# Optimization experiments

Hardware: AMD Instinct MI355X
Metric: run time of the kernel (lower is better)

Reference implementation:

```python
import jax, jax.numpy as jnp
import numpy as np

N, K_, D_ = 16384, 32, 128

def setup_inputs() -> dict:
    key = jax.random.key(0)
    k1, k2, k3 = jax.random.split(key, 3)
    x = jax.random.normal(k1, (1, N, D_), dtype=jnp.float32)
    codes = jax.random.normal(k2, (K_, D_), dtype=jnp.float32)
    scale = jax.random.uniform(k3, (K_,), dtype=jnp.float32)
    return {"x": x, "codes": codes, "scale": scale}

def reference(x, codes, scale):
    # x: (1, N, D) -> residuals R: (N, K, D)
    R = x[0][:, None, :] - codes[None, :, :]
    # scaled L2 norm (NOT squared) over D, scaled per-codeword by `scale`
    l2 = jnp.linalg.norm(R, axis=-1)            # (N, K)
    W = jax.nn.softmax(l2 * scale, axis=-1)     # softmax over K
    # aggregated encoding: (K, D)
    E = jnp.einsum('nk,nkd->kd', W, R)
    return E
```

## Files before the change

kernel.cpp:

```cpp
#include <hip/hip_runtime.h>

constexpr int N    = 16384;
constexpr int K    = 32;
constexpr int D    = 128;
constexpr int SPAD = K + 4;

constexpr int ROWS1 = 32;
constexpr int GRID1 = N / ROWS1;

__global__ __launch_bounds__(256) void enc_partial(
    const float* __restrict__ x,
    const float* __restrict__ codes,
    const float* __restrict__ scale,
    float* __restrict__ ws)
{
    __shared__ float xs[ROWS1][D];
    __shared__ float sc_lds[ROWS1][SPAD];
    __shared__ float w_lds[ROWS1][SPAD];

    const int tid = threadIdx.x;
    const int k   = tid >> 3;
    const int dc  = tid & 7;
    const int d0  = dc << 4;

    {
        const float4* xg = reinterpret_cast<const float4*>(x + (long)blockIdx.x * ROWS1 * D);
        float4* xs4 = reinterpret_cast<float4*>(&xs[0][0]);
        #pragma unroll
        for (int i = 0; i < 4; ++i)
            xs4[tid + i * 256] = xg[tid + i * 256];
    }

    const float4 ck0 = *reinterpret_cast<const float4*>(&codes[k * D + d0 + 0]);
    const float4 ck1 = *reinterpret_cast<const float4*>(&codes[k * D + d0 + 4]);
    const float4 ck2 = *reinterpret_cast<const float4*>(&codes[k * D + d0 + 8]);
    const float4 ck3 = *reinterpret_cast<const float4*>(&codes[k * D + d0 + 12]);
    const float scl = scale[k];

    __syncthreads();

    #pragma unroll 4
    for (int n = 0; n < ROWS1; ++n) {
        const float4* xr = reinterpret_cast<const float4*>(&xs[n][d0]);
        float4 x0 = xr[0], x1 = xr[1], x2 = xr[2], x3 = xr[3];
        float p = 0.f, r;
        r = x0.x - ck0.x; p = fmaf(r, r, p);
        r = x0.y - ck0.y; p = fmaf(r, r, p);
        r = x0.z - ck0.z; p = fmaf(r, r, p);
        r = x0.w - ck0.w; p = fmaf(r, r, p);
        r = x1.x - ck1.x; p = fmaf(r, r, p);
        r = x1.y - ck1.y; p = fmaf(r, r, p);
        r = x1.z - ck1.z; p = fmaf(r, r, p);
        r = x1.w - ck1.w; p = fmaf(r, r, p);
        r = x2.x - ck2.x; p = fmaf(r, r, p);
        r = x2.y - ck2.y; p = fmaf(r, r, p);
        r = x2.z - ck2.z; p = fmaf(r, r, p);
        r = x2.w - ck2.w; p = fmaf(r, r, p);
        r = x3.x - ck3.x; p = fmaf(r, r, p);
        r = x3.y - ck3.y; p = fmaf(r, r, p);
        r = x3.z - ck3.z; p = fmaf(r, r, p);
        r = x3.w - ck3.w; p = fmaf(r, r, p);
        p += __shfl_xor(p, 1);
        p += __shfl_xor(p, 2);
        p += __shfl_xor(p, 4);
        if (dc == 0) sc_lds[n][k] = sqrtf(p) * scl;
    }
    __syncthreads();

    {
        const int row = tid >> 3;
        const int q   = tid & 7;
        float s0 = sc_lds[row][q];
        float s1 = sc_lds[row][q + 8];
        float s2 = sc_lds[row][q + 16];
        float s3 = sc_lds[row][q + 24];
        float m = fmaxf(fmaxf(s0, s1), fmaxf(s2, s3));
        m = fmaxf(m, __shfl_xor(m, 1));
        m = fmaxf(m, __shfl_xor(m, 2));
        m = fmaxf(m, __shfl_xor(m, 4));
        const float LOG2E = 1.44269504088896f;
        float e0 = exp2f((s0 - m) * LOG2E);
        float e1 = exp2f((s1 - m) * LOG2E);
        float e2 = exp2f((s2 - m) * LOG2E);
        float e3 = exp2f((s3 - m) * LOG2E);
        float sum = (e0 + e1) + (e2 + e3);
        sum += __shfl_xor(sum, 1);
        sum += __shfl_xor(sum, 2);
        sum += __shfl_xor(sum, 4);
        float inv = 1.0f / sum;
        w_lds[row][q]      = e0 * inv;
        w_lds[row][q + 8]  = e1 * inv;
        w_lds[row][q + 16] = e2 * inv;
        w_lds[row][q + 24] = e3 * inv;
    }
    __syncthreads();

    float4 t0 = make_float4(0.f, 0.f, 0.f, 0.f);
    float4 t1 = t0, t2 = t0, t3 = t0;
    float sw = 0.f;
    #pragma unroll 4
    for (int n = 0; n < ROWS1; ++n) {
        float w = w_lds[n][k];
        const float4* xr = reinterpret_cast<const float4*>(&xs[n][d0]);
        float4 x0 = xr[0], x1 = xr[1], x2 = xr[2], x3 = xr[3];
        t0.x = fmaf(w, x0.x, t0.x);
        t0.y = fmaf(w, x0.y, t0.y);
        t0.z = fmaf(w, x0.z, t0.z);
        t0.w = fmaf(w, x0.w, t0.w);
        t1.x = fmaf(w, x1.x, t1.x);
        t1.y = fmaf(w, x1.y, t1.y);
        t1.z = fmaf(w, x1.z, t1.z);
        t1.w = fmaf(w, x1.w, t1.w);
        t2.x = fmaf(w, x2.x, t2.x);
        t2.y = fmaf(w, x2.y, t2.y);
        t2.z = fmaf(w, x2.z, t2.z);
        t2.w = fmaf(w, x2.w, t2.w);
        t3.x = fmaf(w, x3.x, t3.x);
        t3.y = fmaf(w, x3.y, t3.y);
        t3.z = fmaf(w, x3.z, t3.z);
        t3.w = fmaf(w, x3.w, t3.w);
        sw += w;
    }

    float* o = ws + (long)blockIdx.x * (K * D) + tid * 16;
    reinterpret_cast<float4*>(o)[0] = make_float4(t0.x - sw * ck0.x, t0.y - sw * ck0.y,
                                                  t0.z - sw * ck0.z, t0.w - sw * ck0.w);
    reinterpret_cast<float4*>(o)[1] = make_float4(t1.x - sw * ck1.x, t1.y - sw * ck1.y,
                                                  t1.z - sw * ck1.z, t1.w - sw * ck1.w);
    reinterpret_cast<float4*>(o)[2] = make_float4(t2.x - sw * ck2.x, t2.y - sw * ck2.y,
                                                  t2.z - sw * ck2.z, t2.w - sw * ck2.w);
    reinterpret_cast<float4*>(o)[3] = make_float4(t3.x - sw * ck3.x, t3.y - sw * ck3.y,
                                                  t3.z - sw * ck3.z, t3.w - sw * ck3.w);
}

__global__ __launch_bounds__(256) void reduce2(
    const float* __restrict__ ws, float* __restrict__ out)
{
    __shared__ float4 part[64][4];

    const int tid   = threadIdx.x;
    const int col   = tid & 3;
    const int slice = tid >> 2;
    const int gcol  = blockIdx.x * 4 + col;

    const float4* P = reinterpret_cast<const float4*>(ws);
    float4 acc = make_float4(0.f, 0.f, 0.f, 0.f);
    #pragma unroll
    for (int r = 0; r < 8; ++r) {
        float4 v = P[(long)(slice * 8 + r) * 1024 + gcol];
        acc.x += v.x; acc.y += v.y; acc.z += v.z; acc.w += v.w;
    }
    part[slice][col] = acc;
    __syncthreads();

    #pragma unroll
    for (int stride = 32; stride >= 1; stride >>= 1) {
        if (slice < stride && col == (tid & 3)) {
            if (tid < stride * 4) {
                float4 a = part[slice][col];
                float4 b = part[slice + stride][col];
                a.x += b.x; a.y += b.y; a.z += b.z; a.w += b.w;
                part[slice][col] = a;
            }
        }
        __syncthreads();
    }
    if (tid < 4) {
        reinterpret_cast<float4*>(out)[blockIdx.x * 4 + tid] = part[0][tid];
    }
}

constexpr int ROWSF = 64;

__global__ __launch_bounds__(256) void enc_atomic(
    const float* __restrict__ x,
    const float* __restrict__ codes,
    const float* __restrict__ scale,
    float* __restrict__ out)
{
    __shared__ float sc_lds[ROWSF][SPAD];
    __shared__ float w_lds[ROWSF][SPAD];

    const int tid = threadIdx.x;
    const int k   = tid >> 3;
    const int dc  = tid & 7;
    const int d0  = dc << 4;

    const float4 ck0 = *reinterpret_cast<const float4*>(&codes[k * D + d0 + 0]);
    const float4 ck1 = *reinterpret_cast<const float4*>(&codes[k * D + d0 + 4]);
    const float4 ck2 = *reinterpret_cast<const float4*>(&codes[k * D + d0 + 8]);
    const float4 ck3 = *reinterpret_cast<const float4*>(&codes[k * D + d0 + 12]);
    const float scl = scale[k];

    const float* xb = x + (long)blockIdx.x * ROWSF * D + d0;

    #pragma unroll 4
    for (int n = 0; n < ROWSF; ++n) {
        const float4* xr = reinterpret_cast<const float4*>(xb + (long)n * D);
        float4 x0 = xr[0], x1 = xr[1], x2 = xr[2], x3 = xr[3];
        float p = 0.f, r;
        r = x0.x - ck0.x; p = fmaf(r, r, p);
        r = x0.y - ck0.y; p = fmaf(r, r, p);
        r = x0.z - ck0.z; p = fmaf(r, r, p);
        r = x0.w - ck0.w; p = fmaf(r, r, p);
        r = x1.x - ck1.x; p = fmaf(r, r, p);
        r = x1.y - ck1.y; p = fmaf(r, r, p);
        r = x1.z - ck1.z; p = fmaf(r, r, p);
        r = x1.w - ck1.w; p = fmaf(r, r, p);
        r = x2.x - ck2.x; p = fmaf(r, r, p);
        r = x2.y - ck2.y; p = fmaf(r, r, p);
        r = x2.z - ck2.z; p = fmaf(r, r, p);
        r = x2.w - ck2.w; p = fmaf(r, r, p);
        r = x3.x - ck3.x; p = fmaf(r, r, p);
        r = x3.y - ck3.y; p = fmaf(r, r, p);
        r = x3.z - ck3.z; p = fmaf(r, r, p);
        r = x3.w - ck3.w; p = fmaf(r, r, p);
        p += __shfl_xor(p, 1);
        p += __shfl_xor(p, 2);
        p += __shfl_xor(p, 4);
        if (dc == 0) sc_lds[n][k] = sqrtf(p) * scl;
    }
    __syncthreads();

    {
        const int row = tid >> 2;
        const int q   = tid & 3;
        float4 s0 = *reinterpret_cast<const float4*>(&sc_lds[row][q * 8 + 0]);
        float4 s1 = *reinterpret_cast<const float4*>(&sc_lds[row][q * 8 + 4]);
        float m = fmaxf(fmaxf(fmaxf(s0.x, s0.y), fmaxf(s0.z, s0.w)),
                        fmaxf(fmaxf(s1.x, s1.y), fmaxf(s1.z, s1.w)));
        m = fmaxf(m, __shfl_xor(m, 1));
        m = fmaxf(m, __shfl_xor(m, 2));
        const float LOG2E = 1.44269504088896f;
        float e0 = exp2f((s0.x - m) * LOG2E);
        float e1 = exp2f((s0.y - m) * LOG2E);
        float e2 = exp2f((s0.z - m) * LOG2E);
        float e3 = exp2f((s0.w - m) * LOG2E);
        float e4 = exp2f((s1.x - m) * LOG2E);
        float e5 = exp2f((s1.y - m) * LOG2E);
        float e6 = exp2f((s1.z - m) * LOG2E);
        float e7 = exp2f((s1.w - m) * LOG2E);
        float sum = ((e0 + e1) + (e2 + e3)) + ((e4 + e5) + (e6 + e7));
        sum += __shfl_xor(sum, 1);
        sum += __shfl_xor(sum, 2);
        float inv = 1.0f / sum;
        *reinterpret_cast<float4*>(&w_lds[row][q * 8 + 0]) =
            make_float4(e0 * inv, e1 * inv, e2 * inv, e3 * inv);
        *reinterpret_cast<float4*>(&w_lds[row][q * 8 + 4]) =
            make_float4(e4 * inv, e5 * inv, e6 * inv, e7 * inv);
    }
    __syncthreads();

    float4 t0 = make_float4(0.f, 0.f, 0.f, 0.f);
    float4 t1 = t0, t2 = t0, t3 = t0;
    float sw = 0.f;
    #pragma unroll 4
    for (int n = 0; n < ROWSF; ++n) {
        float w = w_lds[n][k];
        const float4* xr = reinterpret_cast<const float4*>(xb + (long)n * D);
        float4 x0 = xr[0], x1 = xr[1], x2 = xr[2], x3 = xr[3];
        t0.x = fmaf(w, x0.x, t0.x);
        t0.y = fmaf(w, x0.y, t0.y);
        t0.z = fmaf(w, x0.z, t0.z);
        t0.w = fmaf(w, x0.w, t0.w);
        t1.x = fmaf(w, x1.x, t1.x);
        t1.y = fmaf(w, x1.y, t1.y);
        t1.z = fmaf(w, x1.z, t1.z);
        t1.w = fmaf(w, x1.w, t1.w);
        t2.x = fmaf(w, x2.x, t2.x);
        t2.y = fmaf(w, x2.y, t2.y);
        t2.z = fmaf(w, x2.z, t2.z);
        t2.w = fmaf(w, x2.w, t2.w);
        t3.x = fmaf(w, x3.x, t3.x);
        t3.y = fmaf(w, x3.y, t3.y);
        t3.z = fmaf(w, x3.z, t3.z);
        t3.w = fmaf(w, x3.w, t3.w);
        sw += w;
    }

    float* o = out + k * D + d0;
    atomicAdd(&o[0],  t0.x - sw * ck0.x);
    atomicAdd(&o[1],  t0.y - sw * ck0.y);
    atomicAdd(&o[2],  t0.z - sw * ck0.z);
    atomicAdd(&o[3],  t0.w - sw * ck0.w);
    atomicAdd(&o[4],  t1.x - sw * ck1.x);
    atomicAdd(&o[5],  t1.y - sw * ck1.y);
    atomicAdd(&o[6],  t1.z - sw * ck1.z);
    atomicAdd(&o[7],  t1.w - sw * ck1.w);
    atomicAdd(&o[8],  t2.x - sw * ck2.x);
    atomicAdd(&o[9],  t2.y - sw * ck2.y);
    atomicAdd(&o[10], t2.z - sw * ck2.z);
    atomicAdd(&o[11], t2.w - sw * ck2.w);
    atomicAdd(&o[12], t3.x - sw * ck3.x);
    atomicAdd(&o[13], t3.y - sw * ck3.y);
    atomicAdd(&o[14], t3.z - sw * ck3.z);
    atomicAdd(&o[15], t3.w - sw * ck3.w);
}

extern "C" void kernel_launch(void* const* d_in, const int* in_sizes, int n_in,
                              void* d_out, int out_size, void* d_ws, size_t ws_size,
                              hipStream_t stream) {
    const float* x     = (const float*)d_in[0];
    const float* codes = (const float*)d_in[1];
    const float* scale = (const float*)d_in[2];
    float* out = (float*)d_out;

    const size_t ws_needed = (size_t)GRID1 * K * D * sizeof(float);
    if (ws_size >= ws_needed) {
        float* ws = (float*)d_ws;
        enc_partial<<<GRID1, 256, 0, stream>>>(x, codes, scale, ws);
        reduce2<<<256, 256, 0, stream>>>(ws, out);
    } else {
        hipMemsetAsync(out, 0, K * D * sizeof(float), stream);
        enc_atomic<<<N / ROWSF, 256, 0, stream>>>(x, codes, scale, out);
    }
}
```

Measured before the change: 28.87 us.

## Halve rows per block, drop LDS x staging, split FMA accumulators

Each block now handles 16 rows instead of 32 and reads x directly from global memory (hitting cache) instead of staging it in shared memory, which removes the staging copy and one barrier. The distance computation uses four independent accumulators to shorten the FMA dependency chain. The softmax mapping is adjusted to 16 threads per row, and the reduction kernel sums 16 partials per slice to cover the doubled number of partial blocks. This doubles the partial workspace and the reduce traffic, and each x row is reloaded from cache by all 32 codeword groups.

```diff
diff --git a/kernel.cpp b/kernel.cpp
--- a/kernel.cpp
+++ b/kernel.cpp
@@ -5,7 +5,7 @@
 constexpr int D    = 128;
 constexpr int SPAD = K + 4;
 
-constexpr int ROWS1 = 32;
+constexpr int ROWS1 = 16;
 constexpr int GRID1 = N / ROWS1;
 
 __global__ __launch_bounds__(256) void enc_partial(
@@ -14,7 +14,6 @@
     const float* __restrict__ scale,
     float* __restrict__ ws)
 {
-    __shared__ float xs[ROWS1][D];
     __shared__ float sc_lds[ROWS1][SPAD];
     __shared__ float w_lds[ROWS1][SPAD];
 
@@ -22,14 +21,6 @@
     const int k   = tid >> 3;
     const int dc  = tid & 7;
     const int d0  = dc << 4;
-
-    {
-        const float4* xg = reinterpret_cast<const float4*>(x + (long)blockIdx.x * ROWS1 * D);
-        float4* xs4 = reinterpret_cast<float4*>(&xs[0][0]);
-        #pragma unroll
-        for (int i = 0; i < 4; ++i)
-            xs4[tid + i * 256] = xg[tid + i * 256];
-    }
 
     const float4 ck0 = *reinterpret_cast<const float4*>(&codes[k * D + d0 + 0]);
     const float4 ck1 = *reinterpret_cast<const float4*>(&codes[k * D + d0 + 4]);
@@ -37,29 +28,30 @@
     const float4 ck3 = *reinterpret_cast<const float4*>(&codes[k * D + d0 + 12]);
     const float scl = scale[k];
 
-    __syncthreads();
+    const float* xb = x + (long)blockIdx.x * ROWS1 * D + d0;
 
     #pragma unroll 4
     for (int n = 0; n < ROWS1; ++n) {
-        const float4* xr = reinterpret_cast<const float4*>(&xs[n][d0]);
+        const float4* xr = reinterpret_cast<const float4*>(xb + (long)n * D);
         float4 x0 = xr[0], x1 = xr[1], x2 = xr[2], x3 = xr[3];
-        float p = 0.f, r;
-        r = x0.x - ck0.x; p = fmaf(r, r, p);
-        r = x0.y - ck0.y; p = fmaf(r, r, p);
-        r = x0.z - ck0.z; p = fmaf(r, r, p);
-        r = x0.w - ck0.w; p = fmaf(r, r, p);
-        r = x1.x - ck1.x; p = fmaf(r, r, p);
-        r = x1.y - ck1.y; p = fmaf(r, r, p);
-        r = x1.z - ck1.z; p = fmaf(r, r, p);
-        r = x1.w - ck1.w; p = fmaf(r, r, p);
-        r = x2.x - ck2.x; p = fmaf(r, r, p);
-        r = x2.y - ck2.y; p = fmaf(r, r, p);
-        r = x2.z - ck2.z; p = fmaf(r, r, p);
-        r = x2.w - ck2.w; p = fmaf(r, r, p);
-        r = x3.x - ck3.x; p = fmaf(r, r, p);
-        r = x3.y - ck3.y; p = fmaf(r, r, p);
-        r = x3.z - ck3.z; p = fmaf(r, r, p);
-        r = x3.w - ck3.w; p = fmaf(r, r, p);
+        float p0 = 0.f, p1 = 0.f, p2 = 0.f, p3 = 0.f, r;
+        r = x0.x - ck0.x; p0 = fmaf(r, r, p0);
+        r = x0.y - ck0.y; p1 = fmaf(r, r, p1);
+        r = x0.z - ck0.z; p2 = fmaf(r, r, p2);
+        r = x0.w - ck0.w; p3 = fmaf(r, r, p3);
+        r = x1.x - ck1.x; p0 = fmaf(r, r, p0);
+        r = x1.y - ck1.y; p1 = fmaf(r, r, p1);
+        r = x1.z - ck1.z; p2 = fmaf(r, r, p2);
+        r = x1.w - ck1.w; p3 = fmaf(r, r, p3);
+        r = x2.x - ck2.x; p0 = fmaf(r, r, p0);
+        r = x2.y - ck2.y; p1 = fmaf(r, r, p1);
+        r = x2.z - ck2.z; p2 = fmaf(r, r, p2);
+        r = x2.w - ck2.w; p3 = fmaf(r, r, p3);
+        r = x3.x - ck3.x; p0 = fmaf(r, r, p0);
+        r = x3.y - ck3.y; p1 = fmaf(r, r, p1);
+        r = x3.z - ck3.z; p2 = fmaf(r, r, p2);
+        r = x3.w - ck3.w; p3 = fmaf(r, r, p3);
+        float p = (p0 + p1) + (p2 + p3);
         p += __shfl_xor(p, 1);
         p += __shfl_xor(p, 2);
         p += __shfl_xor(p, 4);
@@ -68,30 +60,26 @@
     __syncthreads();
 
     {
-        const int row = tid >> 3;
-        const int q   = tid & 7;
+        const int row = tid >> 4;
+        const int q   = tid & 15;
         float s0 = sc_lds[row][q];
-        float s1 = sc_lds[row][q + 8];
-        float s2 = sc_lds[row][q + 16];
-        float s3 = sc_lds[row][q + 24];
-        float m = fmaxf(fmaxf(s0, s1), fmaxf(s2, s3));
+        float s1 = sc_lds[row][q + 16];
+        float m = fmaxf(s0, s1);
         m = fmaxf(m, __shfl_xor(m, 1));
         m = fmaxf(m, __shfl_xor(m, 2));
         m = fmaxf(m, __shfl_xor(m, 4));
+        m = fmaxf(m, __shfl_xor(m, 8));
         const float LOG2E = 1.44269504088896f;
         float e0 = exp2f((s0 - m) * LOG2E);
         float e1 = exp2f((s1 - m) * LOG2E);
-        float e2 = exp2f((s2 - m) * LOG2E);
-        float e3 = exp2f((s3 - m) * LOG2E);
-        float sum = (e0 + e1) + (e2 + e3);
+        float sum = e0 + e1;
         sum += __shfl_xor(sum, 1);
         sum += __shfl_xor(sum, 2);
         sum += __shfl_xor(sum, 4);
+        sum += __shfl_xor(sum, 8);
         float inv = 1.0f / sum;
         w_lds[row][q]      = e0 * inv;
-        w_lds[row][q + 8]  = e1 * inv;
-        w_lds[row][q + 16] = e2 * inv;
-        w_lds[row][q + 24] = e3 * inv;
+        w_lds[row][q + 16] = e1 * inv;
     }
     __syncthreads();
 
@@ -101,7 +89,7 @@
     #pragma unroll 4
     for (int n = 0; n < ROWS1; ++n) {
         float w = w_lds[n][k];
-        const float4* xr = reinterpret_cast<const float4*>(&xs[n][d0]);
+        const float4* xr = reinterpret_cast<const float4*>(xb + (long)n * D);
         float4 x0 = xr[0], x1 = xr[1], x2 = xr[2], x3 = xr[3];
         t0.x = fmaf(w, x0.x, t0.x);
         t0.y = fmaf(w, x0.y, t0.y);
@@ -146,8 +134,8 @@
     const float4* P = reinterpret_cast<const float4*>(ws);
     float4 acc = make_float4(0.f, 0.f, 0.f, 0.f);
     #pragma unroll
-    for (int r = 0; r < 8; ++r) {
-        float4 v = P[(long)(slice * 8 + r) * 1024 + gcol];
+    for (int r = 0; r < 16; ++r) {
+        float4 v = P[(long)(slice * 16 + r) * 1024 + gcol];
         acc.x += v.x; acc.y += v.y; acc.z += v.z; acc.w += v.w;
     }
     part[slice][col] = acc;
@@ -155,13 +143,11 @@
 
     #pragma unroll
     for (int stride = 32; stride >= 1; stride >>= 1) {
-        if (slice < stride && col == (tid & 3)) {
-            if (tid < stride * 4) {
-                float4 a = part[slice][col];
-                float4 b = part[slice + stride][col];
-                a.x += b.x; a.y += b.y; a.z += b.z; a.w += b.w;
-                part[slice][col] = a;
-            }
+        if (tid < stride * 4) {
+            float4 a = part[slice][col];
+            float4 b = part[slice + stride][col];
+            a.x += b.x; a.y += b.y; a.z += b.z; a.w += b.w;
+            part[slice][col] = a;
         }
         __syncthreads();
     }
```

After: 49.50 us. +71.5%, slower.
